# Optimization experiments

Measured on AMD Instinct MI355X. Metric: run time of the kernel, lower is better.

The kernel has to match this reference:

```python
import jax, jax.numpy as jnp
import numpy as np

IN_DIM = 128
OUT_DIM = 128
EDGE_DIM = 64
NUM_HEADS = 8
HEAD_DIM = OUT_DIM // NUM_HEADS
N_NODES = 10000
N_EDGES = 320000
LN_EPS = 1e-5


def _gelu(x):
    # torch nn.GELU default is the exact (erf) formulation
    return jax.nn.gelu(x, approximate=False)


def _layernorm(x, g, b):
    mu = jnp.mean(x, axis=-1, keepdims=True)
    var = jnp.var(x, axis=-1, keepdims=True)
    return (x - mu) * jax.lax.rsqrt(var + LN_EPS) * g + b


def setup_inputs() -> dict:
    key = jax.random.key(0)
    ks = jax.random.split(key, 16)

    def lin(k, fan_in, fan_out):
        # torch nn.Linear default init: U(-1/sqrt(fan_in), 1/sqrt(fan_in))
        bound = 1.0 / np.sqrt(fan_in)
        kw, kb = jax.random.split(k)
        w = jax.random.uniform(kw, (fan_in, fan_out), jnp.float32, -bound, bound)
        b = jax.random.uniform(kb, (fan_out,), jnp.float32, -bound, bound)
        return w, b

    node_features = jax.random.normal(ks[0], (N_NODES, IN_DIM), jnp.float32)
    edge_index = jax.random.randint(ks[1], (2, N_EDGES), 0, N_NODES)
    edge_attr = jax.random.normal(ks[2], (N_EDGES, EDGE_DIM), jnp.float32)

    msg_w1, msg_b1 = lin(ks[3], 2 * IN_DIM + EDGE_DIM, OUT_DIM)
    msg_w2, msg_b2 = lin(ks[4], OUT_DIM, OUT_DIM)
    q_w, q_b = lin(ks[5], IN_DIM, OUT_DIM)
    kv_w, kv_b = lin(ks[6], IN_DIM + EDGE_DIM, OUT_DIM)
    out_w1, out_b1 = lin(ks[7], IN_DIM + OUT_DIM, OUT_DIM)
    out_w2, out_b2 = lin(ks[8], OUT_DIM, OUT_DIM)
    ln_g = 1.0 + 0.02 * jax.random.normal(ks[9], (OUT_DIM,), jnp.float32)
    ln_b = 0.02 * jax.random.normal(ks[10], (OUT_DIM,), jnp.float32)

    return dict(node_features=node_features, edge_attr=edge_attr,
                msg_w1=msg_w1, msg_b1=msg_b1, msg_w2=msg_w2, msg_b2=msg_b2,
                q_w=q_w, q_b=q_b, kv_w=kv_w, kv_b=kv_b,
                out_w1=out_w1, out_b1=out_b1, out_w2=out_w2, out_b2=out_b2,
                ln_g=ln_g, ln_b=ln_b, edge_index=edge_index)


def reference(node_features, edge_attr, msg_w1, msg_b1, msg_w2, msg_b2,
              q_w, q_b, kv_w, kv_b, out_w1, out_b1, out_w2, out_b2,
              ln_g, ln_b, edge_index):
    N = node_features.shape[0]
    E = edge_index.shape[1]
    src, dst = edge_index[0], edge_index[1]

    s = node_features[src]                      # [E, Din]
    d = node_features[dst]                      # [E, Din]

    # message MLP
    m_in = jnp.concatenate([s, d, edge_attr], axis=-1)          # [E, 2*Din+De]
    m = _gelu(m_in @ msg_w1 + msg_b1) @ msg_w2 + msg_b2         # [E, Dout]

    # per-edge attention logits
    q = (d @ q_w + q_b).reshape(E, NUM_HEADS, HEAD_DIM)
    kv_in = jnp.concatenate([s, edge_attr], axis=-1)
    kv = (kv_in @ kv_w + kv_b).reshape(E, NUM_HEADS, HEAD_DIM)
    attn = jnp.sum(q * kv, axis=-1) * (HEAD_DIM ** -0.5)        # [E, H]

    # Deterministic version: pick the edge with the largest index per dst node.
    last = jnp.full((N,), -1, dtype=jnp.int32).at[dst].max(
        jnp.arange(E, dtype=jnp.int32))                          # [N]
    attn_full = jnp.where(last[:, None] >= 0,
                          attn[jnp.maximum(last, 0)],
                          -jnp.inf)                              # [N, H]
    # softmax over the NODE axis (dim=0), exactly as the torch code does;
    # -inf rows contribute 0, so using N instead of dst.max()+1 is identical.
    attn_norm = jax.nn.softmax(attn_full, axis=0)[dst]           # [E, H]

    m = (m.reshape(E, NUM_HEADS, HEAD_DIM) * attn_norm[..., None]).reshape(E, OUT_DIM)

    # scatter-add aggregation
    agg = jax.ops.segment_sum(m, dst, num_segments=N)            # [N, Dout]

    h_in = jnp.concatenate([node_features, agg], axis=-1)        # [N, Din+Dout]
    h = _gelu(h_in @ out_w1 + out_b1) @ out_w2 + out_b2          # [N, Dout]

    # res_proj is Identity since in_dim == out_dim; dropout is eval-mode no-op
    return _layernorm(node_features + h, ln_g, ln_b)
```

## Files before the change

### kernel.cpp

```cpp
#include <hip/hip_runtime.h>
#include <hip/hip_bf16.h>

#define NN 10000
#define NE 320000

typedef __bf16 bf16x8 __attribute__((ext_vector_type(8)));
typedef float  f32x4  __attribute__((ext_vector_type(4)));

__device__ __forceinline__ float bf2f(ushort u){
  union { uint i; float f; } c; c.i = ((uint)u) << 16; return c.f;
}
__device__ __forceinline__ ushort f2bf(float f){
  union { float f; uint i; } c; c.f = f;
  uint x = c.i;
  return (ushort)((x + 0x7FFFu + ((x >> 16) & 1u)) >> 16);
}
__device__ __forceinline__ float gelu_erf(float x){
  return 0.5f * x * (1.0f + erff(x * 0.70710678118654752f));
}
__device__ __forceinline__ uint encf(float f){
  uint u = __float_as_uint(f);
  return (u & 0x80000000u) ? ~u : (u | 0x80000000u);
}
__device__ __forceinline__ float decf(uint u){
  return __uint_as_float((u & 0x80000000u) ? (u & 0x7FFFFFFFu) : ~u);
}
#define MFMA16(a,b,c) __builtin_amdgcn_mfma_f32_16x16x32_bf16((a),(b),(c),0,0,0)

__global__ void k_init(const uint* __restrict__ w, int* __restrict__ flag,
                       int* __restrict__ cnt, int* __restrict__ last,
                       uint* __restrict__ Menc, float* __restrict__ S){
  int t = threadIdx.x;
  if (blockIdx.x == 0){
    uint c = 0;
    for (int i = t; i < 4096; i += 256){
      uint v = w[i * 63];
      uint e = (v >> 7) & 0xFF;
      if (e >= 100 && e <= 140) c++;
    }
    __shared__ uint red[256];
    red[t] = c; __syncthreads();
    for (int s = 128; s > 0; s >>= 1){
      if (t < s) red[t] += red[t + s];
      __syncthreads();
    }
    if (t == 0) *flag = (red[0] < 2048) ? 1 : 0;
    return;
  }
  int idx = (blockIdx.x - 1) * 256 + t;
  if (idx < 10000) last[idx] = -1;
  else if (idx < 20000) cnt[idx - 10000] = 0;
  else if (idx < 20008) Menc[idx - 20000] = 0u;
  else if (idx < 20016) S[idx - 20008] = 0.f;
}

__global__ void k_prep(
    const void* NF0, const int* __restrict__ dstI,
    const void* w1, const void* w2, const void* qw, const void* kvw,
    const void* ow1, const void* ow2,
    const void* b1, const void* b2, const void* qb, const void* kvb,
    const void* ob1, const void* ob2, const void* lg, const void* lb,
    int* __restrict__ cnt, int* __restrict__ last,
    ushort* NFc, float* Gagg, ushort* SB, ushort* KVW2,
    ushort* W1aT, ushort* W1bT, ushort* W1cT, ushort* W2T, ushort* QT, ushort* KVT,
    ushort* O1aT, ushort* O1bT, ushort* O2T, const int* flag)
{
  int f = *flag;
  int idx = blockIdx.x * 256 + threadIdx.x;
  if (idx < NE){
    int d = dstI[idx];
    atomicAdd(&cnt[d], 1);
    atomicMax(&last[d], idx);
    return;
  }
  idx -= NE;
  if (idx < 320000){
    if (f){
      float4 v = ((const float4*)NF0)[idx];
      ushort4 o; o.x=f2bf(v.x); o.y=f2bf(v.y); o.z=f2bf(v.z); o.w=f2bf(v.w);
      ((ushort4*)NFc)[idx] = o;
    } else ((ushort4*)NFc)[idx] = ((const ushort4*)NF0)[idx];
    return;
  }
  idx -= 320000;
  if (idx < 320000){ float4 z = {0.f,0.f,0.f,0.f}; ((float4*)Gagg)[idx] = z; return; }
  idx -= 320000;
  if (idx < 1024){
    const void* ps[8] = {b1,b2,qb,kvb,ob1,ob2,lg,lb};
    const void* p = ps[idx >> 7]; int j = idx & 127;
    SB[idx] = f ? f2bf(((const float*)p)[j]) : ((const ushort*)p)[j];
    return;
  }
  idx -= 1024;
  if (idx < 8192){
    KVW2[idx] = f ? f2bf(((const float*)kvw)[16384 + idx]) : ((const ushort*)kvw)[16384 + idx];
    return;
  }
  idx -= 8192;
  if (idx < 16384){ int c=idx>>7,k=idx&127; W1aT[idx] = f? f2bf(((const float*)w1)[k*128+c]) : ((const ushort*)w1)[k*128+c]; return; }
  idx -= 16384;
  if (idx < 16384){ int c=idx>>7,k=idx&127; W1bT[idx] = f? f2bf(((const float*)w1)[(128+k)*128+c]) : ((const ushort*)w1)[(128+k)*128+c]; return; }
  idx -= 16384;
  if (idx < 8192){ int c=idx>>6,k=idx&63;  W1cT[idx] = f? f2bf(((const float*)w1)[(256+k)*128+c]) : ((const ushort*)w1)[(256+k)*128+c]; return; }
  idx -= 8192;
  if (idx < 16384){ int c=idx>>7,k=idx&127; W2T[idx] = f? f2bf(((const float*)w2)[k*128+c]) : ((const ushort*)w2)[k*128+c]; return; }
  idx -= 16384;
  if (idx < 16384){ int c=idx>>7,k=idx&127; QT[idx]  = f? f2bf(((const float*)qw)[k*128+c]) : ((const ushort*)qw)[k*128+c]; return; }
  idx -= 16384;
  if (idx < 16384){ int c=idx>>7,k=idx&127; KVT[idx] = f? f2bf(((const float*)kvw)[k*128+c]) : ((const ushort*)kvw)[k*128+c]; return; }
  idx -= 16384;
  if (idx < 16384){ int c=idx>>7,k=idx&127; O1aT[idx] = f? f2bf(((const float*)ow1)[k*128+c]) : ((const ushort*)ow1)[k*128+c]; return; }
  idx -= 16384;
  if (idx < 16384){ int c=idx>>7,k=idx&127; O1bT[idx] = f? f2bf(((const float*)ow1)[(128+k)*128+c]) : ((const ushort*)ow1)[(128+k)*128+c]; return; }
  idx -= 16384;
  if (idx < 16384){ int c=idx>>7,k=idx&127; O2T[idx] = f? f2bf(((const float*)ow2)[k*128+c]) : ((const ushort*)ow2)[k*128+c]; return; }
}

__global__ __launch_bounds__(1024) void k_scan(const int* __restrict__ cnt,
                                               int* __restrict__ fill){
  __shared__ int sc[1024];
  int t = threadIdx.x;
  int base = t * 10;
  int v[10]; int tot = 0;
  #pragma unroll
  for (int j = 0; j < 10; ++j){
    int idx = base + j;
    v[j] = (idx < NN) ? cnt[idx] : 0;
    tot += v[j];
  }
  sc[t] = tot; __syncthreads();
  for (int off = 1; off < 1024; off <<= 1){
    int x = (t >= off) ? sc[t - off] : 0;
    __syncthreads();
    sc[t] += x;
    __syncthreads();
  }
  int run = sc[t] - tot;
  #pragma unroll
  for (int j = 0; j < 10; ++j){
    int idx = base + j;
    if (idx < NN) fill[idx] = run;
    run += v[j];
  }
}

__global__ __launch_bounds__(256) void k_fillperm(
    const int* __restrict__ srcI, const int* __restrict__ dstI,
    int* __restrict__ fill, int* __restrict__ sSort, int* __restrict__ dSort,
    const float* __restrict__ EAf, const ushort* __restrict__ EAb,
    ushort* __restrict__ EAs,
    const ushort* __restrict__ NFc,
    const ushort* __restrict__ W1aT, const ushort* __restrict__ W1bT,
    const ushort* __restrict__ QT,  const ushort* __restrict__ KVT,
    const ushort* __restrict__ SB,
    ushort* __restrict__ PA, ushort* __restrict__ PB,
    ushort* __restrict__ Qb, ushort* __restrict__ KV1,
    const int* __restrict__ flag)
{
  int t = threadIdx.x;
  if (blockIdx.x >= 1250){
    int l = t & 63, w = t >> 6;
    int m = l & 15, g = l >> 4;
    int row0 = ((int)blockIdx.x - 1250) * 16;
    const ushort* WT = (w==0) ? W1aT : (w==1) ? W1bT : (w==2) ? QT : KVT;
    ushort*       OUT= (w==0) ? PA   : (w==1) ? PB   : (w==2) ? Qb : KV1;
    const f32x4 FZ = {0.f,0.f,0.f,0.f};
    f32x4 acc[8];
    #pragma unroll
    for (int i = 0; i < 8; ++i) acc[i] = FZ;
    int arow = row0 + m;
    #pragma unroll
    for (int ks = 0; ks < 4; ++ks){
      int koff = ks * 32 + g * 8;
      bf16x8 a = *reinterpret_cast<const bf16x8*>(NFc + (size_t)arow * 128 + koff);
      #pragma unroll
      for (int nt = 0; nt < 8; ++nt){
        bf16x8 b = *reinterpret_cast<const bf16x8*>(WT + (size_t)(nt*16+m) * 128 + koff);
        acc[nt] = MFMA16(a, b, acc[nt]);
      }
    }
    #pragma unroll
    for (int nt = 0; nt < 8; ++nt){
      int col = nt * 16 + m;
      float bb = (w==1) ? bf2f(SB[col]) : (w==2) ? bf2f(SB[256+col]) : (w==3) ? bf2f(SB[384+col]) : 0.f;
      #pragma unroll
      for (int r = 0; r < 4; ++r){
        int row = row0 + g * 4 + r;
        OUT[(size_t)row * 128 + col] = f2bf(acc[nt][r] + bb);
      }
    }
    return;
  }
  __shared__ int sp[256];
  int e0 = blockIdx.x * 256;
  int e = e0 + t;
  {
    int d = dstI[e];
    int p = atomicAdd(&fill[d], 1);
    sSort[p] = srcI[e];
    dSort[p] = d;
    sp[t] = p;
  }
  __syncthreads();
  if (*flag){
    #pragma unroll
    for (int pass = 0; pass < 16; ++pass){
      int i = pass * 256 + t;
      int rloc = i >> 4, q = i & 15;
      int p = sp[rloc];
      float4 v = *reinterpret_cast<const float4*>(EAf + (size_t)(e0 + rloc) * 64 + q * 4);
      ushort4 o; o.x=f2bf(v.x); o.y=f2bf(v.y); o.z=f2bf(v.z); o.w=f2bf(v.w);
      *reinterpret_cast<ushort4*>(EAs + (size_t)p * 64 + q * 4) = o;
    }
  } else {
    #pragma unroll
    for (int pass = 0; pass < 8; ++pass){
      int i = pass * 256 + t;
      int rloc = i >> 3, q = i & 7;
      int p = sp[rloc];
      *reinterpret_cast<bf16x8*>(EAs + (size_t)p * 64 + q * 8) =
        *reinterpret_cast<const bf16x8*>(EAb + (size_t)(e0 + rloc) * 64 + q * 8);
    }
  }
}

__global__ __launch_bounds__(256) void k_edgeattn(
    const ushort* __restrict__ PA, const ushort* __restrict__ PB,
    const ushort* __restrict__ EAs,
    const int* __restrict__ sSort, const int* __restrict__ dSort,
    const ushort* __restrict__ W1cT,
    float* __restrict__ Gagg,
    const ushort* __restrict__ Qb, const ushort* __restrict__ KV1,
    const ushort* __restrict__ EAb, const float* __restrict__ EAf,
    const ushort* __restrict__ KVW2,
    const int* __restrict__ srcI, const int* __restrict__ last,
    float* __restrict__ attn, uint* __restrict__ Menc, const int* __restrict__ flag)
{
  __shared__ __align__(16) char Hs[64 * 256];
  __shared__ float LUT[1026];
  __shared__ int sIdx[64], dIdx[64];
  __shared__ int eN[16], sN[16];
  __shared__ uint lmax[8];
  int t = threadIdx.x;

  if (blockIdx.x >= 5000){
    float (*ea_s)[64] = reinterpret_cast<float(*)[64]>(Hs);
    int n0 = ((int)blockIdx.x - 5000) * 16;
    if (t < 16){
      int e = last[n0 + t];
      eN[t] = e;
      sN[t] = (e >= 0) ? srcI[e] : 0;
    }
    if (t < 8) lmax[t] = 0u;
    __syncthreads();
    int F = *flag;
    for (int i = t; i < 1024; i += 256){
      int nn = i >> 6, k = i & 63;
      int e = eN[nn];
      int ee = (e >= 0) ? e : 0;
      float v = F ? EAf[(size_t)ee * 64 + k] : bf2f(EAb[(size_t)ee * 64 + k]);
      ea_s[nn][k] = (e >= 0) ? v : 0.0f;
    }
    __syncthreads();
    int j = t & 127;
    int half = t >> 7;
    float acc[8];
    #pragma unroll
    for (int i = 0; i < 8; ++i) acc[i] = 0.f;
    for (int k = 0; k < 64; ++k){
      float wv = bf2f(KVW2[(size_t)k * 128 + j]);
      #pragma unroll
      for (int nn = 0; nn < 8; ++nn) acc[nn] += ea_s[half * 8 + nn][k] * wv;
    }
    #pragma unroll
    for (int nn = 0; nn < 8; ++nn){
      int nl = half * 8 + nn;
      int n = n0 + nl;
      int e = eN[nl];
      float kvv = acc[nn] + bf2f(KV1[(size_t)sN[nl] * 128 + j]);
      float qv  = bf2f(Qb[(size_t)n * 128 + j]);
      float p = qv * kvv;
      p += __shfl_xor(p, 1); p += __shfl_xor(p, 2);
      p += __shfl_xor(p, 4); p += __shfl_xor(p, 8);
      if ((j & 15) == 0 && e >= 0){
        float v = p * 0.25f;
        attn[(size_t)n * 8 + (j >> 4)] = v;
        atomicMax(&lmax[j >> 4], encf(v));
      }
    }
    __syncthreads();
    if (t < 8 && lmax[t]) atomicMax(&Menc[t], lmax[t]);
    return;
  }

  int p0 = blockIdx.x * 64;
  int l = t & 63, w = t >> 6;
  int m = l & 15, g = l >> 4;

  if (t < 64){ sIdx[t] = sSort[p0 + t]; dIdx[t] = dSort[p0 + t]; }
  for (int i = t; i < 1025; i += 256) LUT[i] = gelu_erf((float)i * (1.0f/64.0f) - 8.0f);
  __syncthreads();

  {
    int r = t >> 2, q = t & 3;
    int sr = sIdx[r], dr = dIdx[r];
    #pragma unroll
    for (int j = 0; j < 4; ++j){
      int c8 = q * 4 + j;
      bf16x8 pa = *reinterpret_cast<const bf16x8*>(PA + (size_t)sr * 128 + c8 * 8);
      bf16x8 pb = *reinterpret_cast<const bf16x8*>(PB + (size_t)dr * 128 + c8 * 8);
      bf16x8 ps;
      #pragma unroll
      for (int k = 0; k < 8; ++k) ps[k] = (__bf16)((float)pa[k] + (float)pb[k]);
      int byte = (r * 256 + c8 * 16) ^ ((r & 7) << 4);
      *reinterpret_cast<bf16x8*>(&Hs[byte]) = ps;
    }
  }

  const f32x4 FZ = {0.f,0.f,0.f,0.f};
  f32x4 acc[8];
  #pragma unroll
  for (int i = 0; i < 8; ++i) acc[i] = FZ;

  #pragma unroll
  for (int ks = 0; ks < 2; ++ks){
    bf16x8 af = *reinterpret_cast<const bf16x8*>(EAs + (size_t)(p0 + w * 16 + m) * 64 + ks * 32 + g * 8);
    #pragma unroll
    for (int nt = 0; nt < 8; ++nt){
      bf16x8 b = *reinterpret_cast<const bf16x8*>(W1cT + (size_t)(nt * 16 + m) * 64 + ks * 32 + g * 8);
      acc[nt] = MFMA16(af, b, acc[nt]);
    }
  }
  __syncthreads();

  #pragma unroll
  for (int nt = 0; nt < 8; ++nt){
    int col = nt * 16 + m;
    #pragma unroll
    for (int r = 0; r < 4; ++r){
      int row = w * 16 + g * 4 + r;
      int byte = (row * 256 + col * 2) ^ ((row & 7) << 4);
      float x = acc[nt][r] + bf2f(*reinterpret_cast<const ushort*>(&Hs[byte]));
      float idxf = fminf(fmaxf((x + 8.0f) * 64.0f, 0.0f), 1023.0f);
      int i = (int)idxf;
      float fr = idxf - (float)i;
      float y = LUT[i] + fr * (LUT[i + 1] - LUT[i]);
      y = (x > 7.9f) ? x : y;
      y = (x < -7.9f) ? 0.0f : y;
      *reinterpret_cast<ushort*>(&Hs[byte]) = f2bf(y);
    }
  }
  __syncthreads();

  {
    int c = t & 127, hh = t >> 7;
    int rS = hh * 32, rE = rS + 32;
    float run = 0.f;
    int cur = dIdx[rS];
    for (int r = rS; r < rE; ++r){
      int d = dIdx[r];
      if (d != cur){
        unsafeAtomicAdd(&Gagg[(size_t)cur * 128 + c], run);
        run = 0.f; cur = d;
      }
      int byte = (r * 256 + c * 2) ^ ((r & 7) << 4);
      run += bf2f(*reinterpret_cast<const ushort*>(&Hs[byte]));
    }
    unsafeAtomicAdd(&Gagg[(size_t)cur * 128 + c], run);
  }
}

__global__ __launch_bounds__(256) void k_asum(
    const float* __restrict__ attn, const int* __restrict__ last,
    const uint* __restrict__ Menc, float* __restrict__ S)
{
  __shared__ float red[256][8];
  int t = threadIdx.x;
  float M[8];
  #pragma unroll
  for (int h = 0; h < 8; ++h) M[h] = decf(Menc[h]);
  float p[8];
  #pragma unroll
  for (int h = 0; h < 8; ++h) p[h] = 0.f;
  for (int n = blockIdx.x * 256 + t; n < NN; n += gridDim.x * 256){
    if (last[n] >= 0){
      #pragma unroll
      for (int h = 0; h < 8; ++h) p[h] += __expf(attn[(size_t)n * 8 + h] - M[h]);
    }
  }
  #pragma unroll
  for (int h = 0; h < 8; ++h) red[t][h] = p[h];
  __syncthreads();
  for (int s = 128; s > 0; s >>= 1){
    if (t < s){
      #pragma unroll
      for (int h = 0; h < 8; ++h) red[t][h] += red[t + s][h];
    }
    __syncthreads();
  }
  if (t < 8) atomicAdd(&S[t], red[0][t]);
}

__global__ __launch_bounds__(256) void k_aggmm2(
    const float* __restrict__ Gagg, const ushort* __restrict__ W2T,
    const ushort* __restrict__ O1aT, const ushort* __restrict__ O1bT,
    const ushort* __restrict__ SB,
    const int* __restrict__ cnt, const int* __restrict__ last,
    const float* __restrict__ attn, const uint* __restrict__ Menc,
    const float* __restrict__ S,
    const ushort* __restrict__ NFc, ushort* __restrict__ T1)
{
  __shared__ __align__(16) char Zs[64 * 256];
  int t = threadIdx.x, l = t & 63, w = t >> 6;
  int m = l & 15, g = l >> 4;
  int row0 = blockIdx.x * 64 + w * 16;

  float M[8], Sinv[8];
  #pragma unroll
  for (int h = 0; h < 8; ++h){ M[h] = decf(Menc[h]); Sinv[h] = 1.0f / S[h]; }

  int arow = row0 + m; if (arow >= NN) arow = NN - 1;
  const f32x4 FZ = {0.f,0.f,0.f,0.f};
  f32x4 acc[8];
  #pragma unroll
  for (int i = 0; i < 8; ++i) acc[i] = FZ;

  #pragma unroll
  for (int ks = 0; ks < 4; ++ks){
    const float* gp = Gagg + (size_t)arow * 128 + ks * 32 + g * 8;
    float4 u0 = *reinterpret_cast<const float4*>(gp);
    float4 u1 = *reinterpret_cast<const float4*>(gp + 4);
    float gv[8] = {u0.x,u0.y,u0.z,u0.w,u1.x,u1.y,u1.z,u1.w};
    bf16x8 hi, lo;
    #pragma unroll
    for (int k = 0; k < 8; ++k){
      hi[k] = (__bf16)gv[k];
      lo[k] = (__bf16)(gv[k] - (float)hi[k]);
    }
    #pragma unroll
    for (int nt = 0; nt < 8; ++nt){
      bf16x8 b = *reinterpret_cast<const bf16x8*>(W2T + (size_t)(nt*16+m) * 128 + ks * 32 + g * 8);
      acc[nt] = MFMA16(hi, b, acc[nt]);
      acc[nt] = MFMA16(lo, b, acc[nt]);
    }
  }

  #pragma unroll
  for (int r = 0; r < 4; ++r){
    int row = row0 + g * 4 + r;
    int rr = (row < NN) ? row : NN - 1;
    float cn = (float)cnt[rr];
    int lst = last[rr];
    int Lr = w * 16 + g * 4 + r;
    #pragma unroll
    for (int nt = 0; nt < 8; ++nt){
      int col = nt * 16 + m;
      float aw = (lst >= 0) ? __expf(attn[(size_t)rr * 8 + nt] - M[nt]) * Sinv[nt] : 0.f;
      float z = (acc[nt][r] + cn * bf2f(SB[128 + col])) * aw;
      int byte = (Lr * 256 + col * 2) ^ ((Lr & 7) << 4);
      *reinterpret_cast<ushort*>(&Zs[byte]) = f2bf(z);
    }
  }
  __syncthreads();

  f32x4 acc2[8];
  #pragma unroll
  for (int i = 0; i < 8; ++i) acc2[i] = FZ;
  int La = w * 16 + m;
  #pragma unroll
  for (int ks = 0; ks < 4; ++ks){
    int koff = ks * 32 + g * 8;
    bf16x8 az = *reinterpret_cast<const bf16x8*>(&Zs[(La * 256 + koff * 2) ^ ((La & 7) << 4)]);
    bf16x8 an = *reinterpret_cast<const bf16x8*>(NFc + (size_t)arow * 128 + koff);
    #pragma unroll
    for (int nt = 0; nt < 8; ++nt){
      bf16x8 b1v = *reinterpret_cast<const bf16x8*>(O1bT + (size_t)(nt*16+m) * 128 + koff);
      bf16x8 b2v = *reinterpret_cast<const bf16x8*>(O1aT + (size_t)(nt*16+m) * 128 + koff);
      acc2[nt] = MFMA16(az, b1v, acc2[nt]);
      acc2[nt] = MFMA16(an, b2v, acc2[nt]);
    }
  }
  #pragma unroll
  for (int nt = 0; nt < 8; ++nt){
    int col = nt * 16 + m;
    float bb = bf2f(SB[512 + col]);
    #pragma unroll
    for (int r = 0; r < 4; ++r){
      int row = row0 + g * 4 + r;
      if (row < NN){
        float v = gelu_erf(acc2[nt][r] + bb);
        T1[(size_t)row * 128 + col] = f2bf(v);
      }
    }
  }
}

__global__ __launch_bounds__(256) void k_out2ln(
    const ushort* __restrict__ T1, const ushort* __restrict__ O2T,
    const ushort* __restrict__ SB,
    const ushort* __restrict__ NFc, void* __restrict__ out,
    const int* __restrict__ flag)
{
  int t = threadIdx.x, l = t & 63, w = t >> 6;
  int m = l & 15, g = l >> 4;
  int row0 = blockIdx.x * 64 + w * 16;
  int F = *flag;
  int arow = row0 + m; if (arow >= NN) arow = NN - 1;
  const f32x4 FZ = {0.f,0.f,0.f,0.f};
  f32x4 acc[8];
  #pragma unroll
  for (int i = 0; i < 8; ++i) acc[i] = FZ;
  #pragma unroll
  for (int ks = 0; ks < 4; ++ks){
    int koff = ks * 32 + g * 8;
    bf16x8 a = *reinterpret_cast<const bf16x8*>(T1 + (size_t)arow * 128 + koff);
    #pragma unroll
    for (int nt = 0; nt < 8; ++nt){
      bf16x8 b = *reinterpret_cast<const bf16x8*>(O2T + (size_t)(nt*16+m) * 128 + koff);
      acc[nt] = MFMA16(a, b, acc[nt]);
    }
  }
  #pragma unroll
  for (int r = 0; r < 4; ++r){
    int row = row0 + g * 4 + r;
    bool ok = row < NN;
    int rr = ok ? row : NN - 1;
    float x[8]; float s = 0.f, q = 0.f;
    #pragma unroll
    for (int nt = 0; nt < 8; ++nt){
      int col = nt * 16 + m;
      float xv = acc[nt][r] + bf2f(SB[640 + col]) + bf2f(NFc[(size_t)rr * 128 + col]);
      x[nt] = xv; s += xv; q += xv * xv;
    }
    #pragma unroll
    for (int msk = 1; msk < 16; msk <<= 1){
      s += __shfl_xor(s, msk);
      q += __shfl_xor(q, msk);
    }
    float mean = s * (1.0f / 128.0f);
    float var  = q * (1.0f / 128.0f) - mean * mean;
    float rs = rsqrtf(var + 1e-5f);
    if (ok){
      #pragma unroll
      for (int nt = 0; nt < 8; ++nt){
        int col = nt * 16 + m;
        float y = (x[nt] - mean) * rs * bf2f(SB[768 + col]) + bf2f(SB[896 + col]);
        if (F) ((float*)out)[(size_t)row * 128 + col] = y;
        else   ((ushort*)out)[(size_t)row * 128 + col] = f2bf(y);
      }
    }
  }
}

extern "C" void kernel_launch(void* const* d_in, const int* in_sizes, int n_in,
                              void* d_out, int out_size, void* d_ws, size_t ws_size,
                              hipStream_t stream)
{
  const void* NF0  = d_in[0];
  const void* EA0  = d_in[1];
  const void* w1   = d_in[2];
  const void* b1   = d_in[3];
  const void* w2   = d_in[4];
  const void* b2   = d_in[5];
  const void* qw   = d_in[6];
  const void* qb   = d_in[7];
  const void* kvw  = d_in[8];
  const void* kvb  = d_in[9];
  const void* ow1  = d_in[10];
  const void* ob1  = d_in[11];
  const void* ow2  = d_in[12];
  const void* ob2  = d_in[13];
  const void* lg   = d_in[14];
  const void* lb   = d_in[15];
  const int*  srcI = (const int*)d_in[16];
  const int*  dstI = srcI + NE;

  char* ws = (char*)d_ws;
  size_t off = 0;
  auto alloc = [&](size_t bytes) -> void* {
    void* p = ws + off;
    off = (off + bytes + 255) & ~(size_t)255;
    return p;
  };
  int*    flag  = (int*)   alloc(4);
  ushort* NFc   = (ushort*)alloc((size_t)NN * 128 * 2);
  ushort* SB    = (ushort*)alloc(8 * 128 * 2);
  ushort* KVW2  = (ushort*)alloc(64 * 128 * 2);
  ushort* W1aT  = (ushort*)alloc(128 * 128 * 2);
  ushort* W1bT  = (ushort*)alloc(128 * 128 * 2);
  ushort* W1cT  = (ushort*)alloc(128 * 64 * 2);
  ushort* W2T   = (ushort*)alloc(128 * 128 * 2);
  ushort* QT    = (ushort*)alloc(128 * 128 * 2);
  ushort* KVT   = (ushort*)alloc(128 * 128 * 2);
  ushort* O1aT  = (ushort*)alloc(128 * 128 * 2);
  ushort* O1bT  = (ushort*)alloc(128 * 128 * 2);
  ushort* O2T   = (ushort*)alloc(128 * 128 * 2);
  int*    last  = (int*)   alloc(NN * 4);
  int*    cnt   = (int*)   alloc(NN * 4);
  int*    fill  = (int*)   alloc(NN * 4);
  int*    sSort = (int*)   alloc((size_t)NE * 4);
  int*    dSort = (int*)   alloc((size_t)NE * 4);
  ushort* EAs   = (ushort*)alloc((size_t)NE * 64 * 2);
  float*  attn  = (float*) alloc(NN * 8 * 4);
  uint*   Menc  = (uint*)  alloc(8 * 4);
  float*  S     = (float*) alloc(8 * 4);
  ushort* PA    = (ushort*)alloc((size_t)NN * 128 * 2);
  ushort* PB    = (ushort*)alloc((size_t)NN * 128 * 2);
  ushort* Qb    = (ushort*)alloc((size_t)NN * 128 * 2);
  ushort* KV1   = (ushort*)alloc((size_t)NN * 128 * 2);
  float*  Gagg  = (float*) alloc((size_t)NN * 128 * 4);
  ushort* T1    = (ushort*)alloc((size_t)NN * 128 * 2);

  k_init<<<80, 256, 0, stream>>>((const uint*)NF0, flag, cnt, last, Menc, S);
  k_prep<<<4330, 256, 0, stream>>>(NF0, dstI, w1, w2, qw, kvw, ow1, ow2,
                                   b1, b2, qb, kvb, ob1, ob2, lg, lb,
                                   cnt, last, NFc, Gagg, SB, KVW2,
                                   W1aT, W1bT, W1cT, W2T, QT, KVT, O1aT, O1bT, O2T, flag);
  k_scan<<<1, 1024, 0, stream>>>(cnt, fill);
  k_fillperm<<<1875, 256, 0, stream>>>(srcI, dstI, fill, sSort, dSort,
                                       (const float*)EA0, (const ushort*)EA0, EAs,
                                       NFc, W1aT, W1bT, QT, KVT, SB,
                                       PA, PB, Qb, KV1, flag);
  k_edgeattn<<<5625, 256, 0, stream>>>(PA, PB, EAs, sSort, dSort, W1cT, Gagg,
                                       Qb, KV1, (const ushort*)EA0, (const float*)EA0,
                                       KVW2, srcI, last, attn, Menc, flag);
  k_asum<<<40, 256, 0, stream>>>(attn, last, Menc, S);
  k_aggmm2<<<157, 256, 0, stream>>>(Gagg, W2T, O1aT, O1bT, SB, cnt, last,
                                    attn, Menc, S, NFc, T1);
  k_out2ln<<<157, 256, 0, stream>>>(T1, O2T, SB, NFc, d_out, flag);
}
```

Measured before the change: 212.7 us.

## Gather edge attributes directly in edge kernel and use tanh GELU

Stops permuting edge_attr into a sorted bf16 buffer in the fill kernel and stores only the original edge index per sorted slot. The edge kernel then gathers each edge's attributes itself (converting from fp32 when needed) into swizzled LDS before the MFMA, which removes one full write and read of the permuted edge-attribute array. It also swaps the LDS lookup-table GELU for a tanh approximation computed with __expf, dropping the LUT build and lookup. The tanh form differs slightly from exact erf GELU, and the gathered reads are now scattered rather than contiguous.

```diff
diff --git a/kernel.cpp b/kernel.cpp
--- a/kernel.cpp
+++ b/kernel.cpp
@@ -17,6 +17,12 @@
 }
 __device__ __forceinline__ float gelu_erf(float x){
   return 0.5f * x * (1.0f + erff(x * 0.70710678118654752f));
+}
+__device__ __forceinline__ float gelu_tanh(float x){
+  float y = 0.7978845608028654f * (x + 0.044715f * x * x * x);
+  float e = __expf(2.f * y);
+  float th = 1.f - 2.f / (e + 1.f);
+  return 0.5f * x * (1.f + th);
 }
 __device__ __forceinline__ uint encf(float f){
   uint u = __float_as_uint(f);
@@ -147,15 +153,13 @@
 __global__ __launch_bounds__(256) void k_fillperm(
     const int* __restrict__ srcI, const int* __restrict__ dstI,
     int* __restrict__ fill, int* __restrict__ sSort, int* __restrict__ dSort,
-    const float* __restrict__ EAf, const ushort* __restrict__ EAb,
-    ushort* __restrict__ EAs,
+    int* __restrict__ eSort,
     const ushort* __restrict__ NFc,
     const ushort* __restrict__ W1aT, const ushort* __restrict__ W1bT,
     const ushort* __restrict__ QT,  const ushort* __restrict__ KVT,
     const ushort* __restrict__ SB,
     ushort* __restrict__ PA, ushort* __restrict__ PB,
-    ushort* __restrict__ Qb, ushort* __restrict__ KV1,
-    const int* __restrict__ flag)
+    ushort* __restrict__ Qb, ushort* __restrict__ KV1)
 {
   int t = threadIdx.x;
   if (blockIdx.x >= 1250){
@@ -191,43 +195,18 @@
     }
     return;
   }
-  __shared__ int sp[256];
-  int e0 = blockIdx.x * 256;
-  int e = e0 + t;
-  {
-    int d = dstI[e];
-    int p = atomicAdd(&fill[d], 1);
-    sSort[p] = srcI[e];
-    dSort[p] = d;
-    sp[t] = p;
-  }
-  __syncthreads();
-  if (*flag){
-    #pragma unroll
-    for (int pass = 0; pass < 16; ++pass){
-      int i = pass * 256 + t;
-      int rloc = i >> 4, q = i & 15;
-      int p = sp[rloc];
-      float4 v = *reinterpret_cast<const float4*>(EAf + (size_t)(e0 + rloc) * 64 + q * 4);
-      ushort4 o; o.x=f2bf(v.x); o.y=f2bf(v.y); o.z=f2bf(v.z); o.w=f2bf(v.w);
-      *reinterpret_cast<ushort4*>(EAs + (size_t)p * 64 + q * 4) = o;
-    }
-  } else {
-    #pragma unroll
-    for (int pass = 0; pass < 8; ++pass){
-      int i = pass * 256 + t;
-      int rloc = i >> 3, q = i & 7;
-      int p = sp[rloc];
-      *reinterpret_cast<bf16x8*>(EAs + (size_t)p * 64 + q * 8) =
-        *reinterpret_cast<const bf16x8*>(EAb + (size_t)(e0 + rloc) * 64 + q * 8);
-    }
-  }
+  int e = blockIdx.x * 256 + t;
+  int d = dstI[e];
+  int p = atomicAdd(&fill[d], 1);
+  sSort[p] = srcI[e];
+  dSort[p] = d;
+  eSort[p] = e;
 }
 
 __global__ __launch_bounds__(256) void k_edgeattn(
     const ushort* __restrict__ PA, const ushort* __restrict__ PB,
-    const ushort* __restrict__ EAs,
     const int* __restrict__ sSort, const int* __restrict__ dSort,
+    const int* __restrict__ eSort,
     const ushort* __restrict__ W1cT,
     float* __restrict__ Gagg,
     const ushort* __restrict__ Qb, const ushort* __restrict__ KV1,
@@ -237,8 +216,8 @@
     float* __restrict__ attn, uint* __restrict__ Menc, const int* __restrict__ flag)
 {
   __shared__ __align__(16) char Hs[64 * 256];
-  __shared__ float LUT[1026];
-  __shared__ int sIdx[64], dIdx[64];
+  __shared__ __align__(16) char EAl[64 * 128];
+  __shared__ int sIdx[64], dIdx[64], eIdx[64];
   __shared__ int eN[16], sN[16];
   __shared__ uint lmax[8];
   int t = threadIdx.x;
@@ -297,12 +276,34 @@
   int l = t & 63, w = t >> 6;
   int m = l & 15, g = l >> 4;
 
-  if (t < 64){ sIdx[t] = sSort[p0 + t]; dIdx[t] = dSort[p0 + t]; }
-  for (int i = t; i < 1025; i += 256) LUT[i] = gelu_erf((float)i * (1.0f/64.0f) - 8.0f);
+  if (t < 64){ sIdx[t] = sSort[p0 + t]; dIdx[t] = dSort[p0 + t]; eIdx[t] = eSort[p0 + t]; }
   __syncthreads();
+  int F = *flag;
 
   {
     int r = t >> 2, q = t & 3;
+    int e = eIdx[r];
+    int kb = q * 32;
+    if (F){
+      const float* src = EAf + (size_t)e * 64 + q * 16;
+      float4 v0 = *reinterpret_cast<const float4*>(src);
+      float4 v1 = *reinterpret_cast<const float4*>(src + 4);
+      float4 v2 = *reinterpret_cast<const float4*>(src + 8);
+      float4 v3 = *reinterpret_cast<const float4*>(src + 12);
+      bf16x8 o0, o1;
+      o0[0]=(__bf16)v0.x; o0[1]=(__bf16)v0.y; o0[2]=(__bf16)v0.z; o0[3]=(__bf16)v0.w;
+      o0[4]=(__bf16)v1.x; o0[5]=(__bf16)v1.y; o0[6]=(__bf16)v1.z; o0[7]=(__bf16)v1.w;
+      o1[0]=(__bf16)v2.x; o1[1]=(__bf16)v2.y; o1[2]=(__bf16)v2.z; o1[3]=(__bf16)v2.w;
+      o1[4]=(__bf16)v3.x; o1[5]=(__bf16)v3.y; o1[6]=(__bf16)v3.z; o1[7]=(__bf16)v3.w;
+      *reinterpret_cast<bf16x8*>(&EAl[(r * 128 + kb)      ^ ((r & 7) << 4)]) = o0;
+      *reinterpret_cast<bf16x8*>(&EAl[(r * 128 + kb + 16) ^ ((r & 7) << 4)]) = o1;
+    } else {
+      const ushort* src = EAb + (size_t)e * 64 + q * 16;
+      *reinterpret_cast<bf16x8*>(&EAl[(r * 128 + kb)      ^ ((r & 7) << 4)]) =
+        *reinterpret_cast<const bf16x8*>(src);
+      *reinterpret_cast<bf16x8*>(&EAl[(r * 128 + kb + 16) ^ ((r & 7) << 4)]) =
+        *reinterpret_cast<const bf16x8*>(src + 8);
+    }
     int sr = sIdx[r], dr = dIdx[r];
     #pragma unroll
     for (int j = 0; j < 4; ++j){
@@ -316,6 +317,7 @@
       *reinterpret_cast<bf16x8*>(&Hs[byte]) = ps;
     }
   }
+  __syncthreads();
 
   const f32x4 FZ = {0.f,0.f,0.f,0.f};
   f32x4 acc[8];
@@ -324,14 +326,14 @@
 
   #pragma unroll
   for (int ks = 0; ks < 2; ++ks){
-    bf16x8 af = *reinterpret_cast<const bf16x8*>(EAs + (size_t)(p0 + w * 16 + m) * 64 + ks * 32 + g * 8);
+    int row = w * 16 + m;
+    bf16x8 af = *reinterpret_cast<const bf16x8*>(&EAl[(row * 128 + ks * 64 + g * 16) ^ ((row & 7) << 4)]);
     #pragma unroll
     for (int nt = 0; nt < 8; ++nt){
       bf16x8 b = *reinterpret_cast<const bf16x8*>(W1cT + (size_t)(nt * 16 + m) * 64 + ks * 32 + g * 8);
       acc[nt] = MFMA16(af, b, acc[nt]);
     }
   }
-  __syncthreads();
 
   #pragma unroll
   for (int nt = 0; nt < 8; ++nt){
@@ -341,13 +343,7 @@
       int row = w * 16 + g * 4 + r;
       int byte = (row * 256 + col * 2) ^ ((row & 7) << 4);
       float x = acc[nt][r] + bf2f(*reinterpret_cast<const ushort*>(&Hs[byte]));
-      float idxf = fminf(fmaxf((x + 8.0f) * 64.0f, 0.0f), 1023.0f);
-      int i = (int)idxf;
-      float fr = idxf - (float)i;
-      float y = LUT[i] + fr * (LUT[i + 1] - LUT[i]);
-      y = (x > 7.9f) ? x : y;
-      y = (x < -7.9f) ? 0.0f : y;
-      *reinterpret_cast<ushort*>(&Hs[byte]) = f2bf(y);
+      *reinterpret_cast<ushort*>(&Hs[byte]) = f2bf(gelu_tanh(x));
     }
   }
   __syncthreads();
@@ -600,7 +596,7 @@
   int*    fill  = (int*)   alloc(NN * 4);
   int*    sSort = (int*)   alloc((size_t)NE * 4);
   int*    dSort = (int*)   alloc((size_t)NE * 4);
-  ushort* EAs   = (ushort*)alloc((size_t)NE * 64 * 2);
+  int*    eSort = (int*)   alloc((size_t)NE * 4);
   float*  attn  = (float*) alloc(NN * 8 * 4);
   uint*   Menc  = (uint*)  alloc(8 * 4);
   float*  S     = (float*) alloc(8 * 4);
@@ -617,11 +613,10 @@
                                    cnt, last, NFc, Gagg, SB, KVW2,
                                    W1aT, W1bT, W1cT, W2T, QT, KVT, O1aT, O1bT, O2T, flag);
   k_scan<<<1, 1024, 0, stream>>>(cnt, fill);
-  k_fillperm<<<1875, 256, 0, stream>>>(srcI, dstI, fill, sSort, dSort,
-                                       (const float*)EA0, (const ushort*)EA0, EAs,
+  k_fillperm<<<1875, 256, 0, stream>>>(srcI, dstI, fill, sSort, dSort, eSort,
                                        NFc, W1aT, W1bT, QT, KVT, SB,
-                                       PA, PB, Qb, KV1, flag);
-  k_edgeattn<<<5625, 256, 0, stream>>>(PA, PB, EAs, sSort, dSort, W1cT, Gagg,
+                                       PA, PB, Qb, KV1);
+  k_edgeattn<<<5625, 256, 0, stream>>>(PA, PB, sSort, dSort, eSort, W1cT, Gagg,
                                        Qb, KV1, (const ushort*)EA0, (const float*)EA0,
                                        KVW2, srcI, last, attn, Menc, flag);
   k_asum<<<40, 256, 0, stream>>>(attn, last, Menc, S);
```

Result: faster. 202.0 us (-5.1%).
